# Performance work log

Hardware: AMD Instinct MI355X
Metric: run time of the kernel (lower is better)

Reference implementation:

```python
import jax, jax.numpy as jnp
import numpy as np


def setup_inputs() -> dict:
    key = jax.random.key(0)
    k1, k2 = jax.random.split(key)
    B, N, M, D = 8, 8192, 8192, 3
    gts = jax.random.normal(k1, (B, N, D), dtype=jnp.float32)
    preds = jax.random.normal(k2, (B, M, D), dtype=jnp.float32)
    return {"gts": gts, "preds": preds}


def reference(gts, preds):
    # Chamfer distance (pytorch3d defaults): squared L2, mean over points,
    # mean over batch, sum of both directions.
    x2 = jnp.sum(gts * gts, axis=-1)          # [B, N]
    y2 = jnp.sum(preds * preds, axis=-1)      # [B, M]
    xy = jnp.einsum('bnd,bmd->bnm', gts, preds)  # [B, N, M]
    d2 = x2[:, :, None] + y2[:, None, :] - 2.0 * xy
    d2 = jnp.maximum(d2, 0.0)  # guard tiny negative values from cancellation
    cham_x = jnp.mean(jnp.min(d2, axis=2))  # x -> nearest y, mean over N then B
    cham_y = jnp.mean(jnp.min(d2, axis=1))  # y -> nearest x, mean over M then B
    return cham_x + cham_y
```

## Files before the change

### kernel.cpp

```cpp
#include <hip/hip_runtime.h>
#include <hip/hip_bf16.h>
#include <math.h>


#define BLOCK 128
#define WAVES 2
#define QPW 64

typedef short short8 __attribute__((ext_vector_type(8)));
typedef float f32x16 __attribute__((ext_vector_type(16)));

union U16S { uint4 v; short8 s; };

__device__ __forceinline__ unsigned int bf16hi(float f) {
    __hip_bfloat16 h = __float2bfloat16(f);
    return (unsigned int)*reinterpret_cast<unsigned short*>(&h);
}
__device__ __forceinline__ float bf16f(unsigned int u) {
    unsigned short us = (unsigned short)u;
    __hip_bfloat16 h;
    *reinterpret_cast<unsigned short*>(&h) = us;
    return __bfloat162float(h);
}

__device__ __forceinline__ f32x16 mfma_bf16(short8 a, short8 b, f32x16 c) {
    f32x16 d;
    asm volatile("v_mfma_f32_32x32x16_bf16 %0, %1, %2, %3"
                 : "=v"(d) : "v"(a), "v"(b), "v"(c));
    return d;
}
__device__ __forceinline__ void mfma_fence(f32x16& a, f32x16& b, f32x16& c, f32x16& d) {
    asm volatile("s_nop 7\n\ts_nop 7" : "+v"(a), "+v"(b), "+v"(c), "+v"(d));
}

__global__ void prep_kernel(const float* __restrict__ gts, const float* __restrict__ preds,
                            int nG, int nP, uint4* __restrict__ RBg, uint4* __restrict__ RBp) {
    const int idx = blockIdx.x * blockDim.x + threadIdx.x;
    if (idx >= nG + nP) return;
    const float* src;
    uint4* dst;
    if (idx < nG) { src = gts + 3 * (size_t)idx;          dst = RBg + 2 * (size_t)idx; }
    else          { src = preds + 3 * (size_t)(idx - nG); dst = RBp + 2 * (size_t)(idx - nG); }
    const float x = src[0], y = src[1], z = src[2];
    const float w = -0.5f * (x * x + y * y + z * z);
    const unsigned int xh = bf16hi(x), yh = bf16hi(y), zh = bf16hi(z), wh = bf16hi(w);
    const unsigned int xl = bf16hi(x - bf16f(xh));
    const unsigned int yl = bf16hi(y - bf16f(yh));
    const unsigned int zl = bf16hi(z - bf16f(zh));
    const unsigned int wl = bf16hi(w - bf16f(wh));
    const unsigned int hx = xh | (yh << 16), hzw = zh | (wh << 16);
    const unsigned int lx = xl | (yl << 16), lzw = zl | (wl << 16);
    dst[0] = make_uint4(hx, hzw, hx, hzw);
    dst[1] = make_uint4(lx, lzw, 0u, 0u);
}

__global__ void __launch_bounds__(BLOCK)
nn_kernel(const uint4* __restrict__ RBg, const uint4* __restrict__ RBp,
          float* __restrict__ partials, int N, int M, int B,
          float invx, float invy) {
    const int z = blockIdx.z;
    const bool dirX = (z < B);
    const int b = dirX ? z : z - B;
    const int NQ = dirX ? N : M;
    const int NR = dirX ? M : N;
    const uint4* Qrb = (dirX ? RBg : RBp) + (size_t)b * NQ * 2;
    const uint4* Rrb = (dirX ? RBp : RBg) + (size_t)b * NR * 2;
    const float inv = dirX ? invx : invy;

    const int tid = threadIdx.x;
    const int lane = tid & 63;
    const int wave = tid >> 6;
    const int m = lane & 31;
    const bool hiK = (lane >= 32);
    const int qBase = (blockIdx.x * WAVES + wave) * QPW;

    __shared__ float sK[WAVES][QPW];
    __shared__ float sPart[WAVES];

    short8 A0s, A1s;
    float wsum0, wsum1;
    {
        const uint4 h0 = Qrb[(size_t)(qBase + m) * 2];
        const uint4 l0 = Qrb[(size_t)(qBase + m) * 2 + 1];
        const uint4 h1 = Qrb[(size_t)(qBase + 32 + m) * 2];
        const uint4 l1 = Qrb[(size_t)(qBase + 32 + m) * 2 + 1];
        U16S a;
        a.v.x = h0.x;
        a.v.y = (h0.y & 0xFFFFu) | 0x3F800000u;
        a.v.z = hiK ? 0u : l0.x;
        a.v.w = hiK ? 0u : (l0.y & 0xFFFFu);
        A0s = a.s;
        a.v.x = h1.x;
        a.v.y = (h1.y & 0xFFFFu) | 0x3F800000u;
        a.v.z = hiK ? 0u : l1.x;
        a.v.w = hiK ? 0u : (l1.y & 0xFFFFu);
        A1s = a.s;
        wsum0 = bf16f(h0.y >> 16) + bf16f(l0.y >> 16);
        wsum1 = bf16f(h1.y >> 16) + bf16f(l1.y >> 16);
    }

    f32x16 zc;
    #pragma unroll
    for (int r = 0; r < 16; ++r) zc[r] = 0.0f;
    f32x16 k0, k1;
    #pragma unroll
    for (int r = 0; r < 16; ++r) { k0[r] = -INFINITY; k1[r] = -INFINITY; }

    const uint4* rp = Rrb + (size_t)m * 2 + (hiK ? 1 : 0);

    auto computeSet = [&](uint4 ta, uint4 tb) {
        U16S ua, ub;
        ua.v = ta; ub.v = tb;
        f32x16 c0 = mfma_bf16(A0s, ua.s, zc);
        f32x16 c1 = mfma_bf16(A1s, ua.s, zc);
        f32x16 c2 = mfma_bf16(A0s, ub.s, zc);
        f32x16 c3 = mfma_bf16(A1s, ub.s, zc);
        mfma_fence(c0, c1, c2, c3);
        #pragma unroll
        for (int r = 0; r < 16; ++r) {
            k0[r] = fmaxf(fmaxf(c0[r], c2[r]), k0[r]);
            k1[r] = fmaxf(fmaxf(c1[r], c3[r]), k1[r]);
        }
    };

    const int nMacro = NR / 128;
    const uint4* p = rp;
    uint4 r0 = p[0], r1 = p[64], r2 = p[128], r3 = p[192];
    uint4 n0, n1, n2, n3;
    for (int i = 0; i < nMacro; i += 2) {
        const uint4* pn = p + 256;
        n0 = pn[0]; n1 = pn[64]; n2 = pn[128]; n3 = pn[192];
        computeSet(r0, r1);
        computeSet(r2, r3);
        const uint4* pn2 = (i + 2 < nMacro) ? (p + 512) : rp;
        r0 = pn2[0]; r1 = pn2[64]; r2 = pn2[128]; r3 = pn2[192];
        computeSet(n0, n1);
        computeSet(n2, n3);
        p += 512;
    }

    #pragma unroll
    for (int r = 0; r < 16; ++r) {
        float v0 = k0[r], v1 = k1[r];
        #pragma unroll
        for (int off = 16; off; off >>= 1) {
            v0 = fmaxf(v0, __shfl_xor(v0, off));
            v1 = fmaxf(v1, __shfl_xor(v1, off));
        }
        if (m == 0) {
            const int row = (r & 3) + 8 * (r >> 2) + 4 * (lane >> 5);
            sK[wave][row] = v0;
            sK[wave][32 + row] = v1;
        }
    }
    const float km = sK[wave][lane];
    const float wsum = hiK ? wsum1 : wsum0;
    const float d2 = fmaxf(-2.0f * (wsum + km), 0.0f);
    float contrib = d2 * inv;
    #pragma unroll
    for (int off = 32; off; off >>= 1) contrib += __shfl_xor(contrib, off);
    if (lane == 0) sPart[wave] = contrib;
    __syncthreads();
    if (tid == 0) {
        float s = 0.0f;
        #pragma unroll
        for (int w = 0; w < WAVES; ++w) s += sPart[w];
        partials[blockIdx.z * gridDim.x + blockIdx.x] = s;
    }
}

__global__ void __launch_bounds__(256)
final_kernel(const float* __restrict__ partials, int n, float* __restrict__ out) {
    float s = 0.0f;
    for (int i = threadIdx.x; i < n; i += 256) s += partials[i];
    #pragma unroll
    for (int off = 32; off; off >>= 1) s += __shfl_xor(s, off);
    __shared__ float ws[4];
    if ((threadIdx.x & 63) == 0) ws[threadIdx.x >> 6] = s;
    __syncthreads();
    if (threadIdx.x == 0) out[0] = ws[0] + ws[1] + ws[2] + ws[3];
}

extern "C" void kernel_launch(void* const* d_in, const int* in_sizes, int n_in,
                              void* d_out, int out_size, void* d_ws, size_t ws_size,
                              hipStream_t stream) {
    const float* gts   = (const float*)d_in[0];
    const float* preds = (const float*)d_in[1];
    float* out = (float*)d_out;

    const int B = 8;
    const int N = in_sizes[0] / (B * 3);
    const int M = in_sizes[1] / (B * 3);
    const int nG = B * N, nP = B * M;

    uint4* RBg = (uint4*)d_ws;
    uint4* RBp = RBg + (size_t)nG * 2;
    float* partials = (float*)(RBp + (size_t)nP * 2);

    prep_kernel<<<(nG + nP + 255) / 256, 256, 0, stream>>>(gts, preds, nG, nP, RBg, RBp);

    const int gx = N / (WAVES * QPW);
    dim3 grid(gx, 1, 2 * B);
    nn_kernel<<<grid, BLOCK, 0, stream>>>(RBg, RBp, partials, N, M, B,
                                          1.0f / (float)nG, 1.0f / (float)nP);

    final_kernel<<<1, 256, 0, stream>>>(partials, 2 * B * gx, out);
}
```

Measured before the change: 101.7 us.

## Split reference set into chunks and merge nearest-neighbor maxima with atomics

Each query block now scans only a quarter of the reference points, with blocks along a new grid dimension covering the other chunks. Per-query maxima are merged through atomicMax on order-preserving integer keys, and a separate reduce kernel applies the norms. Point records shrink to one 16-byte record, and the B operand is built in registers. This raises wave count and occupancy at the cost of global atomics, an extra pass, and a less unrolled inner loop.

After: 114.6 us. 12.7% more time.

```diff
diff --git a/kernel.cpp b/kernel.cpp
--- a/kernel.cpp
+++ b/kernel.cpp
@@ -3,9 +3,10 @@
 #include <math.h>
 
 
-#define BLOCK 128
-#define WAVES 2
+#define BLOCK 256
+#define WAVES 4
 #define QPW 64
+#define NCHUNK 4
 
 typedef short short8 __attribute__((ext_vector_type(8)));
 typedef float f32x16 __attribute__((ext_vector_type(16)));
@@ -22,6 +23,14 @@
     *reinterpret_cast<unsigned short*>(&h) = us;
     return __bfloat162float(h);
 }
+__device__ __forceinline__ unsigned int encodeKey(float f) {
+    unsigned int u = __float_as_uint(f);
+    return (u & 0x80000000u) ? ~u : (u | 0x80000000u);
+}
+__device__ __forceinline__ float decodeKey(unsigned int u) {
+    u = (u & 0x80000000u) ? (u & 0x7FFFFFFFu) : ~u;
+    return __uint_as_float(u);
+}
 
 __device__ __forceinline__ f32x16 mfma_bf16(short8 a, short8 b, f32x16 c) {
     f32x16 d;
@@ -29,18 +38,21 @@
                  : "=v"(d) : "v"(a), "v"(b), "v"(c));
     return d;
 }
-__device__ __forceinline__ void mfma_fence(f32x16& a, f32x16& b, f32x16& c, f32x16& d) {
+__device__ __forceinline__ void mfma_fence4(f32x16& a, f32x16& b, f32x16& c, f32x16& d) {
     asm volatile("s_nop 7\n\ts_nop 7" : "+v"(a), "+v"(b), "+v"(c), "+v"(d));
 }
 
 __global__ void prep_kernel(const float* __restrict__ gts, const float* __restrict__ preds,
-                            int nG, int nP, uint4* __restrict__ RBg, uint4* __restrict__ RBp) {
+                            int nG, int nP, uint4* __restrict__ recG, uint4* __restrict__ recP,
+                            unsigned int* __restrict__ keyAll, float* out) {
     const int idx = blockIdx.x * blockDim.x + threadIdx.x;
+    if (idx == 0) out[0] = 0.0f;
     if (idx >= nG + nP) return;
+    keyAll[idx] = 0u;
     const float* src;
     uint4* dst;
-    if (idx < nG) { src = gts + 3 * (size_t)idx;          dst = RBg + 2 * (size_t)idx; }
-    else          { src = preds + 3 * (size_t)(idx - nG); dst = RBp + 2 * (size_t)(idx - nG); }
+    if (idx < nG) { src = gts + 3 * (size_t)idx;          dst = recG + idx; }
+    else          { src = preds + 3 * (size_t)(idx - nG); dst = recP + (idx - nG); }
     const float x = src[0], y = src[1], z = src[2];
     const float w = -0.5f * (x * x + y * y + z * z);
     const unsigned int xh = bf16hi(x), yh = bf16hi(y), zh = bf16hi(z), wh = bf16hi(w);
@@ -48,56 +60,43 @@
     const unsigned int yl = bf16hi(y - bf16f(yh));
     const unsigned int zl = bf16hi(z - bf16f(zh));
     const unsigned int wl = bf16hi(w - bf16f(wh));
-    const unsigned int hx = xh | (yh << 16), hzw = zh | (wh << 16);
-    const unsigned int lx = xl | (yl << 16), lzw = zl | (wl << 16);
-    dst[0] = make_uint4(hx, hzw, hx, hzw);
-    dst[1] = make_uint4(lx, lzw, 0u, 0u);
-}
-
-__global__ void __launch_bounds__(BLOCK)
-nn_kernel(const uint4* __restrict__ RBg, const uint4* __restrict__ RBp,
-          float* __restrict__ partials, int N, int M, int B,
-          float invx, float invy) {
+    *dst = make_uint4(xh | (yh << 16), zh | (wh << 16),
+                      xl | (yl << 16), zl | (wl << 16));
+}
+
+__global__ void __launch_bounds__(BLOCK, 3)
+nn_kernel(const uint4* __restrict__ recG, const uint4* __restrict__ recP,
+          unsigned int* __restrict__ keyX, unsigned int* __restrict__ keyY,
+          int N, int M, int B) {
     const int z = blockIdx.z;
     const bool dirX = (z < B);
     const int b = dirX ? z : z - B;
     const int NQ = dirX ? N : M;
     const int NR = dirX ? M : N;
-    const uint4* Qrb = (dirX ? RBg : RBp) + (size_t)b * NQ * 2;
-    const uint4* Rrb = (dirX ? RBp : RBg) + (size_t)b * NR * 2;
-    const float inv = dirX ? invx : invy;
+    const uint4* Qr = (dirX ? recG : recP) + (size_t)b * NQ;
+    const uint4* Rr = (dirX ? recP : recG) + (size_t)b * NR;
+    unsigned int* keys = (dirX ? keyX : keyY) + (size_t)b * NQ;
 
     const int tid = threadIdx.x;
     const int lane = tid & 63;
     const int wave = tid >> 6;
     const int m = lane & 31;
-    const bool hiK = (lane >= 32);
+    const bool hiK = lane >= 32;
     const int qBase = (blockIdx.x * WAVES + wave) * QPW;
 
-    __shared__ float sK[WAVES][QPW];
-    __shared__ float sPart[WAVES];
-
-    short8 A0s, A1s;
-    float wsum0, wsum1;
-    {
-        const uint4 h0 = Qrb[(size_t)(qBase + m) * 2];
-        const uint4 l0 = Qrb[(size_t)(qBase + m) * 2 + 1];
-        const uint4 h1 = Qrb[(size_t)(qBase + 32 + m) * 2];
-        const uint4 l1 = Qrb[(size_t)(qBase + 32 + m) * 2 + 1];
-        U16S a;
-        a.v.x = h0.x;
-        a.v.y = (h0.y & 0xFFFFu) | 0x3F800000u;
-        a.v.z = hiK ? 0u : l0.x;
-        a.v.w = hiK ? 0u : (l0.y & 0xFFFFu);
-        A0s = a.s;
-        a.v.x = h1.x;
-        a.v.y = (h1.y & 0xFFFFu) | 0x3F800000u;
-        a.v.z = hiK ? 0u : l1.x;
-        a.v.w = hiK ? 0u : (l1.y & 0xFFFFu);
-        A1s = a.s;
-        wsum0 = bf16f(h0.y >> 16) + bf16f(l0.y >> 16);
-        wsum1 = bf16f(h1.y >> 16) + bf16f(l1.y >> 16);
-    }
+    const uint4 q0 = Qr[qBase + m];
+    const uint4 q1 = Qr[qBase + 32 + m];
+    U16S a;
+    a.v.x = q0.x;
+    a.v.y = (q0.y & 0xFFFFu) | 0x3F800000u;
+    a.v.z = hiK ? 0u : q0.z;
+    a.v.w = hiK ? 0u : (q0.w & 0xFFFFu);
+    const short8 A0 = a.s;
+    a.v.x = q1.x;
+    a.v.y = (q1.y & 0xFFFFu) | 0x3F800000u;
+    a.v.z = hiK ? 0u : q1.z;
+    a.v.w = hiK ? 0u : (q1.w & 0xFFFFu);
+    const short8 A1 = a.s;
 
     f32x16 zc;
     #pragma unroll
@@ -106,37 +105,35 @@
     #pragma unroll
     for (int r = 0; r < 16; ++r) { k0[r] = -INFINITY; k1[r] = -INFINITY; }
 
-    const uint4* rp = Rrb + (size_t)m * 2 + (hiK ? 1 : 0);
-
-    auto computeSet = [&](uint4 ta, uint4 tb) {
-        U16S ua, ub;
-        ua.v = ta; ub.v = tb;
-        f32x16 c0 = mfma_bf16(A0s, ua.s, zc);
-        f32x16 c1 = mfma_bf16(A1s, ua.s, zc);
-        f32x16 c2 = mfma_bf16(A0s, ub.s, zc);
-        f32x16 c3 = mfma_bf16(A1s, ub.s, zc);
-        mfma_fence(c0, c1, c2, c3);
+    const int chunk = NR / NCHUNK;
+    const uint2* rp = (const uint2*)(Rr + (size_t)blockIdx.y * chunk) + 2 * m + (hiK ? 1 : 0);
+    const int iters = chunk / 64;
+
+    uint2 t0 = rp[0], t1 = rp[64];
+    const uint2* p = rp;
+    for (int it = 0; it < iters; ++it) {
+        const uint2* pn = (it + 1 < iters) ? (p + 128) : rp;
+        const uint2 n0 = pn[0];
+        const uint2 n1 = pn[64];
+
+        U16S b0, b1;
+        b0.v.x = t0.x; b0.v.y = t0.y;
+        b0.v.z = hiK ? 0u : t0.x; b0.v.w = hiK ? 0u : t0.y;
+        b1.v.x = t1.x; b1.v.y = t1.y;
+        b1.v.z = hiK ? 0u : t1.x; b1.v.w = hiK ? 0u : t1.y;
+
+        f32x16 c0 = mfma_bf16(A0, b0.s, zc);
+        f32x16 c1 = mfma_bf16(A1, b0.s, zc);
+        f32x16 c2 = mfma_bf16(A0, b1.s, zc);
+        f32x16 c3 = mfma_bf16(A1, b1.s, zc);
+        mfma_fence4(c0, c1, c2, c3);
         #pragma unroll
         for (int r = 0; r < 16; ++r) {
             k0[r] = fmaxf(fmaxf(c0[r], c2[r]), k0[r]);
             k1[r] = fmaxf(fmaxf(c1[r], c3[r]), k1[r]);
         }
-    };
-
-    const int nMacro = NR / 128;
-    const uint4* p = rp;
-    uint4 r0 = p[0], r1 = p[64], r2 = p[128], r3 = p[192];
-    uint4 n0, n1, n2, n3;
-    for (int i = 0; i < nMacro; i += 2) {
-        const uint4* pn = p + 256;
-        n0 = pn[0]; n1 = pn[64]; n2 = pn[128]; n3 = pn[192];
-        computeSet(r0, r1);
-        computeSet(r2, r3);
-        const uint4* pn2 = (i + 2 < nMacro) ? (p + 512) : rp;
-        r0 = pn2[0]; r1 = pn2[64]; r2 = pn2[128]; r3 = pn2[192];
-        computeSet(n0, n1);
-        computeSet(n2, n3);
-        p += 512;
+
+        p = pn; t0 = n0; t1 = n1;
     }
 
     #pragma unroll
@@ -149,36 +146,45 @@
         }
         if (m == 0) {
             const int row = (r & 3) + 8 * (r >> 2) + 4 * (lane >> 5);
-            sK[wave][row] = v0;
-            sK[wave][32 + row] = v1;
-        }
-    }
-    const float km = sK[wave][lane];
-    const float wsum = hiK ? wsum1 : wsum0;
-    const float d2 = fmaxf(-2.0f * (wsum + km), 0.0f);
-    float contrib = d2 * inv;
-    #pragma unroll
-    for (int off = 32; off; off >>= 1) contrib += __shfl_xor(contrib, off);
-    if (lane == 0) sPart[wave] = contrib;
+            atomicMax(&keys[qBase + row], encodeKey(v0));
+            atomicMax(&keys[qBase + 32 + row], encodeKey(v1));
+        }
+    }
+}
+
+__global__ void __launch_bounds__(BLOCK)
+reduce_kernel(const unsigned int* __restrict__ keyX, const float* __restrict__ gts, int nG,
+              const unsigned int* __restrict__ keyY, const float* __restrict__ preds, int nP,
+              float invx, float invy, float* __restrict__ out) {
+    const int total = nG + nP;
+    float local = 0.0f;
+    for (int idx = blockIdx.x * blockDim.x + threadIdx.x; idx < total;
+         idx += gridDim.x * blockDim.x) {
+        if (idx < nG) {
+            const float c = decodeKey(keyX[idx]);
+            const float* q = gts + 3 * (size_t)idx;
+            const float x2 = q[0] * q[0] + q[1] * q[1] + q[2] * q[2];
+            local += fmaxf(x2 - 2.0f * c, 0.0f) * invx;
+        } else {
+            const int j = idx - nG;
+            const float c = decodeKey(keyY[j]);
+            const float* q = preds + 3 * (size_t)j;
+            const float y2 = q[0] * q[0] + q[1] * q[1] + q[2] * q[2];
+            local += fmaxf(y2 - 2.0f * c, 0.0f) * invy;
+        }
+    }
+    __shared__ float waveSums[BLOCK / 64];
+    float v = local;
+    #pragma unroll
+    for (int off = 32; off; off >>= 1) v += __shfl_xor(v, off);
+    if ((threadIdx.x & 63) == 0) waveSums[threadIdx.x >> 6] = v;
     __syncthreads();
-    if (tid == 0) {
+    if (threadIdx.x == 0) {
         float s = 0.0f;
         #pragma unroll
-        for (int w = 0; w < WAVES; ++w) s += sPart[w];
-        partials[blockIdx.z * gridDim.x + blockIdx.x] = s;
-    }
-}
-
-__global__ void __launch_bounds__(256)
-final_kernel(const float* __restrict__ partials, int n, float* __restrict__ out) {
-    float s = 0.0f;
-    for (int i = threadIdx.x; i < n; i += 256) s += partials[i];
-    #pragma unroll
-    for (int off = 32; off; off >>= 1) s += __shfl_xor(s, off);
-    __shared__ float ws[4];
-    if ((threadIdx.x & 63) == 0) ws[threadIdx.x >> 6] = s;
-    __syncthreads();
-    if (threadIdx.x == 0) out[0] = ws[0] + ws[1] + ws[2] + ws[3];
+        for (int w = 0; w < BLOCK / 64; ++w) s += waveSums[w];
+        atomicAdd(out, s);
+    }
 }
 
 extern "C" void kernel_launch(void* const* d_in, const int* in_sizes, int n_in,
@@ -193,16 +199,17 @@
     const int M = in_sizes[1] / (B * 3);
     const int nG = B * N, nP = B * M;
 
-    uint4* RBg = (uint4*)d_ws;
-    uint4* RBp = RBg + (size_t)nG * 2;
-    float* partials = (float*)(RBp + (size_t)nP * 2);
-
-    prep_kernel<<<(nG + nP + 255) / 256, 256, 0, stream>>>(gts, preds, nG, nP, RBg, RBp);
-
-    const int gx = N / (WAVES * QPW);
-    dim3 grid(gx, 1, 2 * B);
-    nn_kernel<<<grid, BLOCK, 0, stream>>>(RBg, RBp, partials, N, M, B,
-                                          1.0f / (float)nG, 1.0f / (float)nP);
-
-    final_kernel<<<1, 256, 0, stream>>>(partials, 2 * B * gx, out);
-}
+    uint4* recG = (uint4*)d_ws;
+    uint4* recP = recG + nG;
+    unsigned int* keyX = (unsigned int*)(recP + nP);
+    unsigned int* keyY = keyX + nG;
+
+    prep_kernel<<<(nG + nP + BLOCK - 1) / BLOCK, BLOCK, 0, stream>>>(
+        gts, preds, nG, nP, recG, recP, keyX, out);
+
+    dim3 grid(N / (WAVES * QPW), NCHUNK, 2 * B);
+    nn_kernel<<<grid, BLOCK, 0, stream>>>(recG, recP, keyX, keyY, N, M, B);
+
+    reduce_kernel<<<(nG + nP + BLOCK - 1) / BLOCK, BLOCK, 0, stream>>>(
+        keyX, gts, nG, keyY, preds, nP, 1.0f / (float)nG, 1.0f / (float)nP, out);
+}
```
